# Optimization experiments

Hardware: AMD Instinct MI355X
Metric: run time of the kernel (lower is better)

## Reference

```python
import jax, jax.numpy as jnp
import numpy as np

NUM_HEADS = 12
EPS = 1e-12  # F.normalize default eps


def setup_inputs() -> dict:
    key = jax.random.key(0)
    ks = jax.random.split(key, 6)
    B, N, C, M = 32, 1024, 768, 64
    s = 1.0 / np.sqrt(C)
    return {
        "x": jax.random.normal(ks[0], (B, N, C), jnp.float32),
        "Wc": jax.random.normal(ks[1], (M, C), jnp.float32) * s,
        "bc": jnp.zeros((M,), jnp.float32),
        "Wq": jax.random.normal(ks[2], (C, C), jnp.float32) * s,
        "bq": jnp.zeros((C,), jnp.float32),
        "Wk": jax.random.normal(ks[3], (C, C), jnp.float32) * s,
        "bk": jnp.zeros((C,), jnp.float32),
        "Wv": jax.random.normal(ks[4], (C, C), jnp.float32) * s,
        "bv": jnp.zeros((C,), jnp.float32),
        "Wp": jax.random.normal(ks[5], (C, C), jnp.float32) * s,
        "bp": jnp.zeros((C,), jnp.float32),
    }


def reference(x, Wc, bc, Wq, bq, Wk, bk, Wv, bv, Wp, bp):
    B, N, C = x.shape
    H = NUM_HEADS
    D = C // H
    scale = D ** -0.5

    # Cluster: linear -> transpose -> sigmoid/N -> einsum -> L2 norm
    c = jnp.einsum('bnc,mc->bmn', x, Wc) + bc[None, :, None]   # (B, M, N)
    c = jax.nn.sigmoid(c) / N
    z = jnp.einsum('bmn,bnc->bmc', c, x)                        # (B, M, C)
    z = z / jnp.maximum(jnp.linalg.norm(z, axis=-1, keepdims=True), EPS)

    M = z.shape[1]
    q = (x @ Wq.T + bq).reshape(B, N, H, D).transpose(0, 2, 1, 3)  # (B,H,N,D)
    k = (z @ Wk.T + bk).reshape(B, M, H, D).transpose(0, 2, 1, 3)  # (B,H,M,D)
    v = (z @ Wv.T + bv).reshape(B, M, H, D).transpose(0, 2, 1, 3)  # (B,H,M,D)

    attn = jax.nn.softmax(jnp.einsum('bhnd,bhmd->bhnm', q, k) * scale, axis=-1)
    o = jnp.einsum('bhnm,bhmd->bhnd', attn, v)                  # (B,H,N,D)
    o = o.transpose(0, 2, 1, 3).reshape(B, N, C)
    return o @ Wp.T + bp
```

## Files before the change

kernel.cpp:

```cpp
#include <hip/hip_runtime.h>
#include <hip/hip_bf16.h>
#include <cstdint>

#define BB 32
#define NN 1024
#define CC 768
#define MM 64
#define HH 12
#define DD 64

typedef float f4v __attribute__((ext_vector_type(4)));
typedef __bf16 bf8 __attribute__((ext_vector_type(8)));
typedef __bf16 bf4 __attribute__((ext_vector_type(4)));

__device__ __forceinline__ f4v mfma16(bf8 a, bf8 b, f4v c) {
    return __builtin_amdgcn_mfma_f32_16x16x32_bf16(a, b, c, 0, 0, 0);
}
__device__ __forceinline__ __bf16 f2bf(float f) { return (__bf16)f; }

__device__ __forceinline__ void gl2lds16(const void* g, void* lds) {
    __builtin_amdgcn_global_load_lds((const __attribute__((address_space(1))) void*)g,
                                     (__attribute__((address_space(3))) void*)lds, 16, 0, 0);
}


__global__ __launch_bounds__(256) void k_cvtW(
        const float* __restrict__ Wc, const float* __restrict__ Wq,
        const float* __restrict__ Wk, const float* __restrict__ Wv,
        const float* __restrict__ Wp,
        __bf16* __restrict__ wc, __bf16* __restrict__ wq,
        __bf16* __restrict__ wk, __bf16* __restrict__ wv,
        __bf16* __restrict__ wp) {
    const float* in; __bf16* out; int n4; int frag;
    switch (blockIdx.y) {
        case 0: in = Wc; out = wc; n4 = MM * CC / 4; frag = 1; break;
        case 1: in = Wq; out = wq; n4 = CC * CC / 4; frag = 1; break;
        case 2: in = Wk; out = wk; n4 = CC * CC / 4; frag = 0; break;
        case 3: in = Wv; out = wv; n4 = CC * CC / 4; frag = 0; break;
        default: in = Wp; out = wp; n4 = CC * CC / 4; frag = 1; break;
    }
    int i = blockIdx.x * 256 + threadIdx.x;
    if (i < n4) {
        float4 v = *(const float4*)&in[i * 4];
        bf4 o; o[0] = f2bf(v.x); o[1] = f2bf(v.y); o[2] = f2bf(v.z); o[3] = f2bf(v.w);
        if (frag) {
            int lin = i * 4, m = lin / CC, c = lin % CC;
            size_t off = ((size_t)((m >> 4) * 24 + (c >> 5))) * 512
                       + ((((c >> 3) & 3) * 16) + (m & 15)) * 8 + (c & 7);
            *(bf4*)&out[off] = o;
        } else {
            *(bf4*)&out[i * 4] = o;
        }
    }
}

__global__ __launch_bounds__(256) void k_cvtx(const float* __restrict__ x,
        __bf16* __restrict__ xb, __bf16* __restrict__ xt) {
    int c0 = blockIdx.x * 64, n0 = blockIdx.y * 64, b = blockIdx.z;
    __shared__ __align__(16) __bf16 tileT[64 * 66];
    __shared__ __align__(16) __bf16 tileR[64 * 72];
    int t = threadIdx.x;
#pragma unroll
    for (int i = 0; i < 4; i++) {
        int idx = t + 256 * i, r = idx >> 4, cq = idx & 15;
        float4 v = *(const float4*)&x[((size_t)(b * NN + n0 + r)) * CC + c0 + cq * 4];
        float vv[4] = {v.x, v.y, v.z, v.w};
        bf4 o;
#pragma unroll
        for (int j = 0; j < 4; j++) {
            __bf16 bv = f2bf(vv[j]);
            o[j] = bv;
            tileT[(cq * 4 + j) * 66 + r] = bv;
        }
        *(bf4*)&tileR[r * 72 + cq * 4] = o;
    }
    __syncthreads();
    int gnt = b * 64 + (n0 >> 4);
    int kc0 = c0 >> 5;
    int lane = t & 63;
#pragma unroll
    for (int i = 0; i < 2; i++) {
        int idx = t + 256 * i;
        int nt_loc = idx >> 7, kc_loc = (idx >> 6) & 1;
        int row = nt_loc * 16 + (lane & 15);
        int col = kc_loc * 32 + (lane >> 4) * 8;
        bf8 v = *(const bf8*)&tileR[row * 72 + col];
        *(bf8*)&xb[((size_t)((gnt + nt_loc) * 24 + kc0 + kc_loc)) * 512 + lane * 8] = v;
    }
#pragma unroll
    for (int i = 0; i < 2; i++) {
        int idx = t + 256 * i, c = idx >> 3, ch = idx & 7;
        bf8 v2 = *(const bf8*)&tileT[c * 66 + ch * 8];
        *(bf8*)&xt[((size_t)(b * CC + c0 + c)) * NN + n0 + ch * 8] = v2;
    }
}

__global__ __launch_bounds__(256) void k_cluster(const __bf16* __restrict__ xb,
        const __bf16* __restrict__ Wc, const float* __restrict__ bc,
        __bf16* __restrict__ cbmn) {
    int n0 = blockIdx.x * 128, b = blockIdx.y;
    int t = threadIdx.x, w = t >> 6, l = t & 63, quad = (l >> 4), l16 = l & 15;
    int nt0 = b * 64 + (n0 >> 4);
    f4v acc[2][4];
#pragma unroll
    for (int i = 0; i < 2; i++) for (int j = 0; j < 4; j++) acc[i][j] = (f4v)0.0f;
    for (int kc = 0; kc < 24; kc++) {
        bf8 afr[2], bfr[4];
#pragma unroll
        for (int sr = 0; sr < 2; sr++)
            afr[sr] = *(const bf8*)&xb[((size_t)((nt0 + w * 2 + sr) * 24 + kc)) * 512 + l * 8];
#pragma unroll
        for (int sc = 0; sc < 4; sc++)
            bfr[sc] = *(const bf8*)&Wc[((size_t)(sc * 24 + kc)) * 512 + l * 8];
#pragma unroll
        for (int sr = 0; sr < 2; sr++)
#pragma unroll
            for (int sc = 0; sc < 4; sc++)
                acc[sr][sc] = mfma16(afr[sr], bfr[sc], acc[sr][sc]);
    }
#pragma unroll
    for (int sr = 0; sr < 2; sr++)
#pragma unroll
        for (int sc = 0; sc < 4; sc++) {
            int m = sc * 16 + l16;
            float bias = bc[m];
            bf4 p;
#pragma unroll
            for (int r = 0; r < 4; r++) {
                float val = acc[sr][sc][r] + bias;
                val = 1.0f / (1.0f + __expf(-val));
                p[r] = f2bf(val * (1.0f / 1024.0f));
            }
            *(bf4*)&cbmn[((size_t)(b * MM + m)) * NN + n0 + w * 32 + sr * 16 + quad * 4] = p;
        }
}

__global__ __launch_bounds__(256) void k_z(const __bf16* __restrict__ cbmn,
        const __bf16* __restrict__ xt, float* __restrict__ z) {
    int c0 = blockIdx.x * 64, b = blockIdx.y;
    int t = threadIdx.x, w = t >> 6, l = t & 63, quad = l >> 4, l16 = l & 15;
    f4v acc[4];
#pragma unroll
    for (int j = 0; j < 4; j++) acc[j] = (f4v)0.0f;
    for (int n0 = 0; n0 < NN; n0 += 32) {
        bf8 afr = *(const bf8*)&cbmn[((size_t)(b * MM + w * 16 + l16)) * NN + n0 + quad * 8];
#pragma unroll
        for (int sc = 0; sc < 4; sc++) {
            bf8 bfr = *(const bf8*)&xt[((size_t)(b * CC + c0 + sc * 16 + l16)) * NN + n0 + quad * 8];
            acc[sc] = mfma16(afr, bfr, acc[sc]);
        }
    }
#pragma unroll
    for (int sc = 0; sc < 4; sc++) {
        int cc = c0 + sc * 16 + l16;
#pragma unroll
        for (int r = 0; r < 4; r++) {
            int m = w * 16 + quad * 4 + r;
            z[((size_t)(b * MM + m)) * CC + cc] = acc[sc][r];
        }
    }
}

__global__ __launch_bounds__(256) void k_znorm(const float* __restrict__ z, __bf16* __restrict__ zb) {
    int w = threadIdx.x >> 6, l = threadIdx.x & 63;
    int row = blockIdx.x * 4 + w;
    const float* zr = &z[(size_t)row * CC];
    float v[12]; float ss = 0.f;
#pragma unroll
    for (int i = 0; i < 12; i++) { v[i] = zr[l + i * 64]; ss += v[i] * v[i]; }
#pragma unroll
    for (int off = 32; off; off >>= 1) ss += __shfl_xor(ss, off);
    float s = 1.0f / fmaxf(sqrtf(ss), 1e-12f);
    __bf16* zo = &zb[(size_t)row * CC];
#pragma unroll
    for (int i = 0; i < 12; i++) zo[l + i * 64] = f2bf(v[i] * s);
}

__global__ __launch_bounds__(256) void k_kv(const __bf16* __restrict__ zb,
        const __bf16* __restrict__ Wk, const float* __restrict__ bk,
        const __bf16* __restrict__ Wv, const float* __restrict__ bv,
        __bf16* __restrict__ kout, __bf16* __restrict__ vtout) {
    int ct = blockIdx.x, b = blockIdx.y, which = blockIdx.z;
    const __bf16* W = which ? Wv : Wk;
    const float* bias = which ? bv : bk;
    int t = threadIdx.x, w = t >> 6, l = t & 63, quad = l >> 4, l16 = l & 15;
    f4v acc[4][2];
#pragma unroll
    for (int i = 0; i < 4; i++) for (int j = 0; j < 2; j++) acc[i][j] = (f4v)0.0f;
    for (int k0 = 0; k0 < CC; k0 += 32) {
        bf8 afr[4], bfr[2];
#pragma unroll
        for (int sr = 0; sr < 4; sr++)
            afr[sr] = *(const bf8*)&zb[((size_t)(b * MM + sr * 16 + l16)) * CC + k0 + quad * 8];
#pragma unroll
        for (int sc = 0; sc < 2; sc++)
            bfr[sc] = *(const bf8*)&W[((size_t)(ct * 128 + w * 32 + sc * 16 + l16)) * CC + k0 + quad * 8];
#pragma unroll
        for (int sr = 0; sr < 4; sr++)
#pragma unroll
            for (int sc = 0; sc < 2; sc++)
                acc[sr][sc] = mfma16(afr[sr], bfr[sc], acc[sr][sc]);
    }
#pragma unroll
    for (int sr = 0; sr < 4; sr++)
#pragma unroll
        for (int sc = 0; sc < 2; sc++) {
            int col = ct * 128 + w * 32 + sc * 16 + l16;
            float bb = bias[col];
            int h = col >> 6, d = col & 63;
            if (which == 0) {
#pragma unroll
                for (int r = 0; r < 4; r++) {
                    int m = sr * 16 + quad * 4 + r;
                    kout[(((size_t)(b * HH + h)) * MM + m) * DD + d] = f2bf(acc[sr][sc][r] + bb);
                }
            } else {
                bf4 p;
#pragma unroll
                for (int r = 0; r < 4; r++) p[r] = f2bf(acc[sr][sc][r] + bb);
                *(bf4*)&vtout[(((size_t)(b * HH + h)) * DD + d) * MM + sr * 16 + quad * 4] = p;
            }
        }
}

#define STAGE_AF(Asrc, buf, kcs)                                                      \
    do {                                                                              \
        __bf16* _d = (buf);                                                           \
        gl2lds16(&(Asrc)[((size_t)((gt0 + w) * 24 + (kcs))) * 512 + l * 8], &_d[w * 512]); \
        gl2lds16(&(Asrc)[((size_t)((gt0 + w + 4) * 24 + (kcs))) * 512 + l * 8], &_d[(w + 4) * 512]); \
    } while (0)

#define GEMM_KLOOP_H(Asrc, Bsrc)                                                      \
    bf8 bcur[4], bnxt[4];                                                             \
    _Pragma("unroll")                                                                 \
    for (int sc = 0; sc < 4; sc++)                                                    \
        bcur[sc] = *(const bf8*)&(Bsrc)[((size_t)((jt * 16 + w * 4 + sc) * 24)) * 512 + l * 8]; \
    STAGE_AF(Asrc, As3, 0);                                                           \
    STAGE_AF(Asrc, As3 + 4096, 1);                                                    \
    asm volatile("s_waitcnt vmcnt(2)" ::: "memory");                                  \
    __builtin_amdgcn_s_barrier();                                                     \
    for (int kt = 0; kt < 24; ++kt) {                                                 \
        const __bf16* As = As3 + (kt % 3) * 4096;                                     \
        if (kt < 23) {                                                                \
            _Pragma("unroll")                                                         \
            for (int sc = 0; sc < 4; sc++)                                            \
                bnxt[sc] = *(const bf8*)&(Bsrc)[((size_t)((jt * 16 + w * 4 + sc) * 24 + kt + 1)) * 512 + l * 8]; \
        }                                                                             \
        bf8 afr[8];                                                                   \
        _Pragma("unroll")                                                             \
        for (int sr = 0; sr < 8; sr++)                                                \
            afr[sr] = *(const bf8*)&As[sr * 512 + l * 8];                             \
        __builtin_amdgcn_sched_barrier(0);                                            \
        if (kt < 22) STAGE_AF(Asrc, As3 + ((kt + 2) % 3) * 4096, kt + 2);             \
        __builtin_amdgcn_s_setprio(1);                                                \
        _Pragma("unroll")                                                             \
        for (int sr = 0; sr < 8; sr++)                                                \
            _Pragma("unroll")                                                         \
            for (int sc = 0; sc < 4; sc++)                                            \
                acc[sr][sc] = mfma16(afr[sr], bcur[sc], acc[sr][sc]);                 \
        __builtin_amdgcn_s_setprio(0);                                                \
        if (kt < 23) {                                                                \
            _Pragma("unroll")                                                         \
            for (int sc = 0; sc < 4; sc++) bcur[sc] = bnxt[sc];                       \
        }                                                                             \
        if (kt < 22)       asm volatile("s_waitcnt vmcnt(6)" ::: "memory");           \
        else if (kt == 22) asm volatile("s_waitcnt vmcnt(4)" ::: "memory");           \
        __builtin_amdgcn_s_barrier();                                                 \
    }

__global__ __launch_bounds__(256, 2) void k_qproj(const __bf16* __restrict__ xb,
        const __bf16* __restrict__ Wq, const float* __restrict__ bq,
        __bf16* __restrict__ qb) {
    int orig = blockIdx.x;
    int lid = (orig & 7) * 96 + (orig >> 3);
    int jt = lid % 3;
    int gt0 = (lid / 3) * 8;

    __shared__ __align__(16) __bf16 As3[3 * 4096];
    int t = threadIdx.x, w = t >> 6, l = t & 63, quad = l >> 4, l16 = l & 15;
    f4v acc[8][4];
#pragma unroll
    for (int i = 0; i < 8; i++) for (int j = 0; j < 4; j++) acc[i][j] = (f4v)0.0f;

    GEMM_KLOOP_H(xb, Wq);

    __bf16* eb = As3;
    for (int p = 0; p < 4; ++p) {
        if (w == p) {
#pragma unroll
            for (int sc = 0; sc < 4; sc++) {
                int col = jt * 256 + p * 64 + sc * 16 + l16;
                float bb = bq[col];
#pragma unroll
                for (int sr = 0; sr < 8; sr++)
#pragma unroll
                    for (int r = 0; r < 4; r++)
                        eb[(sr * 16 + quad * 4 + r) * 72 + sc * 16 + l16] = f2bf(acc[sr][sc][r] + bb);
            }
        }
        __syncthreads();
        int h = jt * 4 + p;
#pragma unroll
        for (int i = 0; i < 4; i++) {
            int idx = t + 256 * i, nt = idx >> 7, kcs = (idx >> 6) & 1, lane = idx & 63;
            bf8 v = *(const bf8*)&eb[(nt * 16 + (lane & 15)) * 72 + kcs * 32 + (lane >> 4) * 8];
            *(bf8*)&qb[((size_t)(((gt0 + nt) * 12 + h) * 2 + kcs)) * 512 + lane * 8] = v;
        }
        __syncthreads();
    }
}

#define QS 72
__global__ __launch_bounds__(256) void k_attn(const __bf16* __restrict__ qb,
        const __bf16* __restrict__ kb, const __bf16* __restrict__ vt,
        __bf16* __restrict__ ob) {
    int n0 = blockIdx.x * 128, h = blockIdx.y, b = blockIdx.z;
    __shared__ __align__(16) __bf16 ps[128 * QS];
    int t = threadIdx.x, w = t >> 6, l = t & 63, quad = l >> 4, l16 = l & 15;
    size_t bh = (size_t)(b * HH + h);
    int nt0 = b * 64 + (n0 >> 4);

    f4v sacc[2][4];
#pragma unroll
    for (int i = 0; i < 2; i++) for (int j = 0; j < 4; j++) sacc[i][j] = (f4v)0.0f;
#pragma unroll
    for (int kc = 0; kc < 2; kc++) {
        bf8 afr[2], bfr[4];
#pragma unroll
        for (int sr = 0; sr < 2; sr++)
            afr[sr] = *(const bf8*)&qb[((size_t)(((nt0 + w * 2 + sr) * 12 + h) * 2 + kc)) * 512 + l * 8];
#pragma unroll
        for (int sc = 0; sc < 4; sc++)
            bfr[sc] = *(const bf8*)&kb[(bh * MM + sc * 16 + l16) * DD + kc * 32 + quad * 8];
#pragma unroll
        for (int sr = 0; sr < 2; sr++)
#pragma unroll
            for (int sc = 0; sc < 4; sc++)
                sacc[sr][sc] = mfma16(afr[sr], bfr[sc], sacc[sr][sc]);
    }
#pragma unroll
    for (int sr = 0; sr < 2; sr++) {
#pragma unroll
        for (int r = 0; r < 4; r++) {
            float mx = -1e30f;
#pragma unroll
            for (int sc = 0; sc < 4; sc++) mx = fmaxf(mx, sacc[sr][sc][r] * 0.125f);
#pragma unroll
            for (int off = 1; off < 16; off <<= 1) mx = fmaxf(mx, __shfl_xor(mx, off));
            float e[4]; float sum = 0.f;
#pragma unroll
            for (int sc = 0; sc < 4; sc++) { e[sc] = __expf(sacc[sr][sc][r] * 0.125f - mx); sum += e[sc]; }
#pragma unroll
            for (int off = 1; off < 16; off <<= 1) sum += __shfl_xor(sum, off);
            float inv = 1.0f / sum;
            int row = w * 32 + sr * 16 + quad * 4 + r;
#pragma unroll
            for (int sc = 0; sc < 4; sc++) ps[row * QS + sc * 16 + l16] = f2bf(e[sc] * inv);
        }
    }
    f4v oacc[2][4];
#pragma unroll
    for (int i = 0; i < 2; i++) for (int j = 0; j < 4; j++) oacc[i][j] = (f4v)0.0f;
#pragma unroll
    for (int kc = 0; kc < 2; kc++) {
        bf8 afr[2], bfr[4];
#pragma unroll
        for (int sr = 0; sr < 2; sr++)
            afr[sr] = *(const bf8*)&ps[(w * 32 + sr * 16 + l16) * QS + kc * 32 + quad * 8];
#pragma unroll
        for (int sc = 0; sc < 4; sc++)
            bfr[sc] = *(const bf8*)&vt[(bh * DD + sc * 16 + l16) * MM + kc * 32 + quad * 8];
#pragma unroll
        for (int sr = 0; sr < 2; sr++)
#pragma unroll
            for (int sc = 0; sc < 4; sc++)
                oacc[sr][sc] = mfma16(afr[sr], bfr[sc], oacc[sr][sc]);
    }
#pragma unroll
    for (int sr = 0; sr < 2; sr++)
#pragma unroll
        for (int sc = 0; sc < 4; sc++) {
            int row = w * 32 + sr * 16;
#pragma unroll
            for (int r = 0; r < 4; r++)
                ps[(row + quad * 4 + r) * QS + sc * 16 + l16] = f2bf(oacc[sr][sc][r]);
        }
    __syncthreads();
#pragma unroll
    for (int i = 0; i < 4; i++) {
        int idx = t + 256 * i, nt = idx >> 7, kcs = (idx >> 6) & 1, lane = idx & 63;
        bf8 v = *(const bf8*)&ps[(nt * 16 + (lane & 15)) * QS + kcs * 32 + (lane >> 4) * 8];
        *(bf8*)&ob[((size_t)((nt0 + nt) * 24 + h * 2 + kcs)) * 512 + lane * 8] = v;
    }
}

__global__ __launch_bounds__(256, 2) void k_oproj(const __bf16* __restrict__ ob,
        const __bf16* __restrict__ Wp, const float* __restrict__ bp,
        float* __restrict__ out) {
    int orig = blockIdx.x;
    int lid = (orig & 7) * 96 + (orig >> 3);
    int jt = lid % 3;
    int gt0 = (lid / 3) * 8;
    size_t arow0 = (size_t)(lid / 3) * 128;

    __shared__ __align__(16) __bf16 As3[17408];
    int t = threadIdx.x, w = t >> 6, l = t & 63, quad = l >> 4, l16 = l & 15;
    f4v acc[8][4];
#pragma unroll
    for (int i = 0; i < 8; i++) for (int j = 0; j < 4; j++) acc[i][j] = (f4v)0.0f;

    GEMM_KLOOP_H(ob, Wp);

    float* ebf = (float*)As3;
    for (int p = 0; p < 4; ++p) {
        if (w == p) {
#pragma unroll
            for (int sc = 0; sc < 4; sc++) {
                int col = jt * 256 + p * 64 + sc * 16 + l16;
                float bb = bp[col];
#pragma unroll
                for (int sr = 0; sr < 8; sr++)
#pragma unroll
                    for (int r = 0; r < 4; r++)
                        ebf[(sr * 16 + quad * 4 + r) * 68 + sc * 16 + l16] = acc[sr][sc][r] + bb;
            }
        }
        __syncthreads();
#pragma unroll
        for (int i = 0; i < 8; i++) {
            int idx = t + 256 * i, row = idx >> 4, c4 = idx & 15;
            *(float4*)&out[(arow0 + row) * CC + jt * 256 + p * 64 + c4 * 4] = *(const float4*)&ebf[row * 68 + c4 * 4];
        }
        __syncthreads();
    }
}

extern "C" void kernel_launch(void* const* d_in, const int* in_sizes, int n_in,
                              void* d_out, int out_size, void* d_ws, size_t ws_size,
                              hipStream_t stream) {
    (void)in_sizes; (void)n_in; (void)out_size; (void)ws_size;
    const float* x  = (const float*)d_in[0];
    const float* Wc = (const float*)d_in[1];
    const float* bc = (const float*)d_in[2];
    const float* Wq = (const float*)d_in[3];
    const float* bq = (const float*)d_in[4];
    const float* Wk = (const float*)d_in[5];
    const float* bk = (const float*)d_in[6];
    const float* Wv = (const float*)d_in[7];
    const float* bv = (const float*)d_in[8];
    const float* Wp = (const float*)d_in[9];
    const float* bp = (const float*)d_in[10];
    float* out = (float*)d_out;

    char* ws = (char*)d_ws;
    size_t off = 0;
    auto alloc = [&](size_t bytes) { void* p = ws + off; off = (off + bytes + 255) & ~(size_t)255; return p; };
    __bf16* wc_b = (__bf16*)alloc((size_t)MM * CC * 2);
    __bf16* wq_b = (__bf16*)alloc((size_t)CC * CC * 2);
    __bf16* wk_b = (__bf16*)alloc((size_t)CC * CC * 2);
    __bf16* wv_b = (__bf16*)alloc((size_t)CC * CC * 2);
    __bf16* wp_b = (__bf16*)alloc((size_t)CC * CC * 2);
    __bf16* xb   = (__bf16*)alloc((size_t)BB * NN * CC * 2);
    __bf16* xt_o = (__bf16*)alloc((size_t)BB * NN * CC * 2);
    __bf16* q_b  = (__bf16*)alloc((size_t)BB * NN * CC * 2);
    __bf16* c_bmn= (__bf16*)alloc((size_t)BB * MM * NN * 2);
    float*  z_f  = (float*) alloc((size_t)BB * MM * CC * 4);
    __bf16* z_b  = (__bf16*)alloc((size_t)BB * MM * CC * 2);
    __bf16* k_b  = (__bf16*)alloc((size_t)BB * HH * MM * DD * 2);
    __bf16* v_t  = (__bf16*)alloc((size_t)BB * HH * MM * DD * 2);

    k_cvtW<<<dim3((CC * CC / 4 + 255) / 256, 5), 256, 0, stream>>>(
        Wc, Wq, Wk, Wv, Wp, wc_b, wq_b, wk_b, wv_b, wp_b);

    k_cvtx<<<dim3(CC / 64, NN / 64, BB), 256, 0, stream>>>(x, xb, xt_o);
    k_cluster<<<dim3(NN / 128, BB), 256, 0, stream>>>(xb, wc_b, bc, c_bmn);
    k_z<<<dim3(CC / 64, BB), 256, 0, stream>>>(c_bmn, xt_o, z_f);
    k_znorm<<<(BB * MM) / 4, 256, 0, stream>>>(z_f, z_b);
    k_kv<<<dim3(CC / 128, BB, 2), 256, 0, stream>>>(z_b, wk_b, bk, wv_b, bv, k_b, v_t);
    k_qproj<<<dim3((BB * NN / 128) * 3), 256, 0, stream>>>(xb, wq_b, bq, q_b);
    k_attn<<<dim3(NN / 128, HH, BB), 256, 0, stream>>>(q_b, k_b, v_t, xt_o );
    k_oproj<<<dim3((BB * NN / 128) * 3), 256, 0, stream>>>(xt_o, wp_b, bp, out);
}
```

Measured before the change: 265.1 us.

## Store K and V in MFMA fragment-packed layout via LDS transpose

```diff
diff --git a/kernel.cpp b/kernel.cpp
--- a/kernel.cpp
+++ b/kernel.cpp
@@ -183,7 +183,9 @@
     int ct = blockIdx.x, b = blockIdx.y, which = blockIdx.z;
     const __bf16* W = which ? Wv : Wk;
     const float* bias = which ? bv : bk;
+    __shared__ __align__(16) __bf16 tile[128 * 72];
     int t = threadIdx.x, w = t >> 6, l = t & 63, quad = l >> 4, l16 = l & 15;
+    int h0 = ct * 2;
     f4v acc[4][2];
 #pragma unroll
     for (int i = 0; i < 4; i++) for (int j = 0; j < 2; j++) acc[i][j] = (f4v)0.0f;
@@ -205,22 +207,33 @@
     for (int sr = 0; sr < 4; sr++)
 #pragma unroll
         for (int sc = 0; sc < 2; sc++) {
-            int col = ct * 128 + w * 32 + sc * 16 + l16;
-            float bb = bias[col];
-            int h = col >> 6, d = col & 63;
-            if (which == 0) {
-#pragma unroll
-                for (int r = 0; r < 4; r++) {
-                    int m = sr * 16 + quad * 4 + r;
-                    kout[(((size_t)(b * HH + h)) * MM + m) * DD + d] = f2bf(acc[sr][sc][r] + bb);
-                }
-            } else {
-                bf4 p;
-#pragma unroll
-                for (int r = 0; r < 4; r++) p[r] = f2bf(acc[sr][sc][r] + bb);
-                *(bf4*)&vtout[(((size_t)(b * HH + h)) * DD + d) * MM + sr * 16 + quad * 4] = p;
+            int col = w * 32 + sc * 16 + l16;
+            float bb = bias[ct * 128 + col];
+#pragma unroll
+            for (int r = 0; r < 4; r++) {
+                int m = sr * 16 + quad * 4 + r;
+                __bf16 val = f2bf(acc[sr][sc][r] + bb);
+                if (which == 0) tile[m * 136 + col] = val;
+                else            tile[col * 72 + m] = val;
             }
         }
+    __syncthreads();
+#pragma unroll
+    for (int i = 0; i < 4; i++) {
+        int idx = t + 256 * i;
+        int bid = idx >> 6, lane = idx & 63;
+        int h_loc = bid >> 3, t4 = (bid >> 1) & 3, kc2 = bid & 1;
+        int h = h0 + h_loc;
+        if (which == 0) {
+            int m = t4 * 16 + (lane & 15), d = kc2 * 32 + (lane >> 4) * 8;
+            bf8 v = *(const bf8*)&tile[m * 136 + h_loc * 64 + d];
+            *(bf8*)&kout[((size_t)(((b * HH + h) * 4 + t4) * 2 + kc2)) * 512 + lane * 8] = v;
+        } else {
+            int d = t4 * 16 + (lane & 15), m = kc2 * 32 + (lane >> 4) * 8;
+            bf8 v = *(const bf8*)&tile[(h_loc * 64 + d) * 72 + m];
+            *(bf8*)&vtout[((size_t)(((b * HH + h) * 4 + t4) * 2 + kc2)) * 512 + lane * 8] = v;
+        }
+    }
 }
 
 #define STAGE_AF(Asrc, buf, kcs)                                                      \
@@ -331,7 +344,7 @@
             afr[sr] = *(const bf8*)&qb[((size_t)(((nt0 + w * 2 + sr) * 12 + h) * 2 + kc)) * 512 + l * 8];
 #pragma unroll
         for (int sc = 0; sc < 4; sc++)
-            bfr[sc] = *(const bf8*)&kb[(bh * MM + sc * 16 + l16) * DD + kc * 32 + quad * 8];
+            bfr[sc] = *(const bf8*)&kb[((size_t)((bh * 4 + sc) * 2 + kc)) * 512 + l * 8];
 #pragma unroll
         for (int sr = 0; sr < 2; sr++)
 #pragma unroll
@@ -369,7 +382,7 @@
             afr[sr] = *(const bf8*)&ps[(w * 32 + sr * 16 + l16) * QS + kc * 32 + quad * 8];
 #pragma unroll
         for (int sc = 0; sc < 4; sc++)
-            bfr[sc] = *(const bf8*)&vt[(bh * DD + sc * 16 + l16) * MM + kc * 32 + quad * 8];
+            bfr[sc] = *(const bf8*)&vt[((size_t)((bh * 4 + sc) * 2 + kc)) * 512 + l * 8];
 #pragma unroll
         for (int sr = 0; sr < 2; sr++)
 #pragma unroll
```

After: 258.7 us. -2.4%, faster.
